# Kernel tuning notes

Measured on AMD Instinct MI355X. Metric: run time of the kernel, lower is better.

## Reference

```python
import jax, jax.numpy as jnp
import numpy as np

KH = KW = 3
K = KH * KW
GROUPS = 8


def conv_same(x, w, b=None):
    out = jax.lax.conv_general_dilated(x, w, (1, 1), 'SAME',
                                       dimension_numbers=('NHWC', 'HWIO', 'NHWC'))
    if b is not None:
        out = out + b
    return out


def feature_selection(x, w_att, w_sel):
    pooled = x.mean(axis=(1, 2), keepdims=True)            # [B,1,1,C]
    attn = jax.nn.sigmoid(conv_same(pooled, w_att))        # 1x1 conv, sigmoid
    return conv_same(x * (attn + 1.0), w_sel)              # [B,H,W,F]


def deform_sample(x, sy, sx):
    # x: [H,W,G,Cg]; sy,sx: [H,W,G,K] fractional sample coords (zero outside)
    H, W, G, _ = x.shape
    y0 = jnp.floor(sy)
    x0 = jnp.floor(sx)
    wy1 = sy - y0
    wx1 = sx - x0
    gi = jnp.arange(G)[None, None, :, None]

    def gather(yi, xi):
        valid = (yi >= 0) & (yi <= H - 1) & (xi >= 0) & (xi <= W - 1)
        yc = jnp.clip(yi, 0, H - 1).astype(jnp.int32)
        xc = jnp.clip(xi, 0, W - 1).astype(jnp.int32)
        v = x[yc, xc, gi]                                   # [H,W,G,K,Cg]
        return v * valid[..., None]

    v00 = gather(y0, x0)
    v01 = gather(y0, x0 + 1)
    v10 = gather(y0 + 1, x0)
    v11 = gather(y0 + 1, x0 + 1)
    wy1 = wy1[..., None]
    wx1 = wx1[..., None]
    top = v00 * (1 - wx1) + v01 * wx1
    bot = v10 * (1 - wx1) + v11 * wx1
    return top * (1 - wy1) + bot * wy1                      # [H,W,G,K,Cg]


def dcnv2(x, align, w_om, b_om, w_dcn, b_dcn):
    # x: [B,H,W,C] input to deform-conv; align: [B,H,W,Ca] alignment feature
    B, H, W, C = x.shape
    G = GROUPS
    Cg = C // G
    om = conv_same(align, w_om, b_om)                       # [B,H,W,G*3*K]
    off = om[..., :G * 2 * K].reshape(B, H, W, G, K, 2)     # (dy, dx)
    mask = jax.nn.sigmoid(om[..., G * 2 * K:]).reshape(B, H, W, G, K)

    iy = jnp.arange(H, dtype=x.dtype)[:, None, None, None]
    ix = jnp.arange(W, dtype=x.dtype)[None, :, None, None]
    ky, kx = jnp.meshgrid(jnp.arange(KH) - (KH - 1) // 2,
                          jnp.arange(KW) - (KW - 1) // 2, indexing='ij')
    ky = ky.reshape(K).astype(x.dtype)
    kx = kx.reshape(K).astype(x.dtype)
    sy = iy + ky + off[..., 0]                              # [B,H,W,G,K]
    sx = ix + kx + off[..., 1]

    xg = x.reshape(B, H, W, G, Cg)
    sampled = jax.vmap(deform_sample)(xg, sy, sx)           # [B,H,W,G,K,Cg]
    sampled = sampled * mask[..., None]
    sampled = sampled.transpose(0, 1, 2, 4, 3, 5).reshape(B, H, W, K, C)
    wk = w_dcn.reshape(K, C, -1)                            # [K,C,F]
    return jnp.einsum('bhwkc,kcf->bhwf', sampled, wk) + b_dcn


def reference(coarse, fine, w_att, w_sel, w_off, w_om, b_om, w_dcn, b_dcn):
    B, H, W, _ = fine.shape
    coarse_up = jax.image.resize(coarse, (B, H, W, coarse.shape[-1]), 'bilinear')
    fine_cal = feature_selection(fine, w_att, w_sel)
    fc = jnp.concatenate([fine_cal, coarse_up * 2.0], axis=-1)
    align = conv_same(fc, w_off)                            # 1x1, no bias
    aligned = jax.nn.relu(dcnv2(coarse_up, align, w_om, b_om, w_dcn, b_dcn))
    return aligned + fine_cal


def setup_inputs() -> dict:
    key = jax.random.key(0)
    ks = jax.random.split(key, 8)
    B, H, W = 4, 64, 64
    Cc, Cf, F = 256, 256, 256
    s = lambda fan: (2.0 / fan) ** 0.5
    return {
        'coarse': jax.random.normal(ks[0], (B, H // 2, W // 2, Cc), jnp.float32),
        'fine': jax.random.normal(ks[1], (B, H, W, Cf), jnp.float32),
        'w_att': jax.random.normal(ks[2], (1, 1, Cf, Cf), jnp.float32) * s(Cf),
        'w_sel': jax.random.normal(ks[3], (1, 1, Cf, F), jnp.float32) * s(Cf),
        'w_off': jax.random.normal(ks[4], (1, 1, F + Cc, 2 * F), jnp.float32) * s(F + Cc),
        'w_om': jax.random.normal(ks[5], (3, 3, 2 * F, GROUPS * 3 * K), jnp.float32) * 0.01,
        'b_om': jnp.zeros((GROUPS * 3 * K,), jnp.float32),
        'w_dcn': jax.random.normal(ks[6], (3, 3, Cc, F), jnp.float32) * s(9 * Cc),
        'b_dcn': jnp.zeros((F,), jnp.float32),
    }
```

## Files before the change

### kernel.cpp

```cpp
#include <hip/hip_runtime.h>
#include <hip/hip_bf16.h>
#include <cstddef>

constexpr int HWP = 64 * 64;
constexpr int CCH = 256;
constexpr int OMC = 216;
constexpr int KDC = 2304;

typedef __attribute__((ext_vector_type(8))) short bf16x8;
typedef __attribute__((ext_vector_type(4))) float f32x4;

__device__ inline unsigned short f2bf(float x) {
  __hip_bfloat16 h = __float2bfloat16(x);
  return *reinterpret_cast<unsigned short*>(&h);
}
__device__ inline float bf2f(unsigned short u) {
  unsigned int v = ((unsigned int)u) << 16;
  return __uint_as_float(v);
}
__device__ inline void bfpair(unsigned int u, float& a, float& b) {
  a = __uint_as_float(u << 16);
  b = __uint_as_float(u & 0xffff0000u);
}

__global__ __launch_bounds__(256) void prep_weights(
    const float* __restrict__ w_off, const float* __restrict__ w_om,
    const float* __restrict__ w_sel, const float* __restrict__ w_dcn,
    unsigned short* __restrict__ w_offT, unsigned short* __restrict__ w_omT,
    unsigned short* __restrict__ w_selT, unsigned short* __restrict__ w_dcnT) {
  int i = blockIdx.x * 256 + threadIdx.x;
  if (i < 512 * 512) {
    int n = i >> 9, k = i & 511;
    w_offT[i] = f2bf(w_off[k * 512 + n]);
  }
  if (i < 9 * 224 * 512) {
    int c = i & 511;
    int r = i >> 9;
    int tap = r / 224;
    int n = r - tap * 224;
    w_omT[i] = f2bf(n < OMC ? w_om[((size_t)tap * 512 + c) * OMC + n] : 0.f);
  }
  if (i < 256 * 256) {
    int n = i >> 8, k = i & 255;
    w_selT[i] = f2bf(w_sel[k * 256 + n]);
  }
  if (i < 9 * 256 * 256) {
    int tap = i >> 16, f = (i >> 8) & 255, c = i & 255;
    w_dcnT[i] = f2bf(w_dcn[((size_t)tap * 256 + c) * 256 + f]);
  }
}

__global__ __launch_bounds__(256) void pool_partial(
    const float* __restrict__ fine, float* __restrict__ partial) {
  int r = blockIdx.x;
  int b = blockIdx.y;
  int t = threadIdx.x;
  const float* src = fine + ((size_t)b * 4096 + r * 64) * 256 + t;
  float s = 0.f;
#pragma unroll 8
  for (int p = 0; p < 64; ++p) s += src[(size_t)p * 256];
  partial[((size_t)b * 64 + r) * 256 + t] = s;
}

__global__ __launch_bounds__(256) void pool_finish(
    const float* __restrict__ partial, const float* __restrict__ w_att,
    float* __restrict__ scale) {
  __shared__ float pl[256];
  int b = blockIdx.x;
  int t = threadIdx.x;
  const float* pp = partial + (size_t)b * 64 * 256 + t;
  float s = 0.f;
#pragma unroll 8
  for (int r = 0; r < 64; ++r) s += pp[(size_t)r * 256];
  pl[t] = s * (1.0f / 4096.0f);
  __syncthreads();
  float acc = 0.f;
  for (int ci = 0; ci < 256; ++ci) acc += pl[ci] * w_att[ci * 256 + t];
  scale[b * 256 + t] = 1.0f + 1.0f / (1.0f + expf(-acc));
}

__global__ __launch_bounds__(256) void upsample_kernel(
    const float* __restrict__ coarse, unsigned short* __restrict__ upbf,
    unsigned short* __restrict__ alignA) {
  int m = blockIdx.x;
  int c = threadIdx.x;
  int b = m >> 12, h = (m >> 6) & 63, w = m & 63;
  float cy = fminf(fmaxf(h * 0.5f - 0.25f, 0.f), 31.f);
  float cx = fminf(fmaxf(w * 0.5f - 0.25f, 0.f), 31.f);
  int y0 = (int)cy, x0 = (int)cx;
  float fy = cy - y0, fx = cx - x0;
  int y1 = min(y0 + 1, 31), x1 = min(x0 + 1, 31);
  const float* base = coarse + (size_t)b * 32 * 32 * CCH;
  float v00 = base[(y0 * 32 + x0) * CCH + c];
  float v01 = base[(y0 * 32 + x1) * CCH + c];
  float v10 = base[(y1 * 32 + x0) * CCH + c];
  float v11 = base[(y1 * 32 + x1) * CCH + c];
  float top = v00 + (v01 - v00) * fx;
  float bot = v10 + (v11 - v10) * fx;
  float v = top + (bot - top) * fy;
  upbf[(size_t)m * CCH + c] = f2bf(v);
  alignA[(size_t)m * 512 + 256 + c] = f2bf(2.f * v);
}

__global__ __launch_bounds__(256) void gemm_finecal_mfma(
    const float* __restrict__ fine, const float* __restrict__ scale,
    const unsigned short* __restrict__ w_selT,
    float* __restrict__ finecal, unsigned short* __restrict__ alignA) {
  __shared__ unsigned short As[128][72];
  __shared__ unsigned short Bs[64][72];
  __shared__ float sc[256];
  int n0 = blockIdx.x * 64;
  int m0 = blockIdx.y * 128;
  int t = threadIdx.x;
  int wid = t >> 6, lane = t & 63;
  int lrow = lane & 15, lq = lane >> 4;
  int bb = m0 >> 12;
  sc[t] = scale[bb * 256 + t];
  f32x4 acc[2][4];
#pragma unroll
  for (int i = 0; i < 2; ++i)
#pragma unroll
    for (int j = 0; j < 4; ++j) acc[i][j] = (f32x4){0.f, 0.f, 0.f, 0.f};
  for (int k0 = 0; k0 < 256; k0 += 64) {
    __syncthreads();
    for (int u = t; u < 128 * 8; u += 256) {
      int row = u >> 3, ck = u & 7;
      const float* fp = &fine[(size_t)(m0 + row) * 256 + k0 + ck * 8];
      float4 f0 = *(const float4*)fp;
      float4 f1 = *(const float4*)(fp + 4);
      int kb = k0 + ck * 8;
      ushort4 u0 = make_ushort4(f2bf(f0.x * sc[kb]), f2bf(f0.y * sc[kb + 1]),
                                f2bf(f0.z * sc[kb + 2]), f2bf(f0.w * sc[kb + 3]));
      ushort4 u1 = make_ushort4(f2bf(f1.x * sc[kb + 4]), f2bf(f1.y * sc[kb + 5]),
                                f2bf(f1.z * sc[kb + 6]), f2bf(f1.w * sc[kb + 7]));
      *(ushort4*)&As[row][ck * 8] = u0;
      *(ushort4*)&As[row][ck * 8 + 4] = u1;
    }
    for (int u = t; u < 64 * 8; u += 256) {
      int row = u >> 3, ck = u & 7;
      *(uint4*)&Bs[row][ck * 8] = *(const uint4*)&w_selT[(size_t)(n0 + row) * 256 + k0 + ck * 8];
    }
    __syncthreads();
#pragma unroll
    for (int kk = 0; kk < 2; ++kk) {
      bf16x8 a[2], b[4];
#pragma unroll
      for (int mt = 0; mt < 2; ++mt)
        a[mt] = *(const bf16x8*)&As[wid * 32 + mt * 16 + lrow][kk * 32 + lq * 8];
#pragma unroll
      for (int nt = 0; nt < 4; ++nt)
        b[nt] = *(const bf16x8*)&Bs[nt * 16 + lrow][kk * 32 + lq * 8];
#pragma unroll
      for (int mt = 0; mt < 2; ++mt)
#pragma unroll
        for (int nt = 0; nt < 4; ++nt)
          acc[mt][nt] = __builtin_amdgcn_mfma_f32_16x16x32_bf16(
              a[mt], b[nt], acc[mt][nt], 0, 0, 0);
    }
  }
#pragma unroll
  for (int mt = 0; mt < 2; ++mt)
#pragma unroll
    for (int nt = 0; nt < 4; ++nt)
#pragma unroll
      for (int r = 0; r < 4; ++r) {
        int m = m0 + wid * 32 + mt * 16 + lq * 4 + r;
        int n = n0 + nt * 16 + lrow;
        finecal[(size_t)m * 256 + n] = acc[mt][nt][r];
        alignA[(size_t)m * 512 + n] = f2bf(acc[mt][nt][r]);
      }
}

__global__ __launch_bounds__(256) void gemm_align_mfma(
    const unsigned short* __restrict__ alignA,
    const unsigned short* __restrict__ w_offT,
    unsigned short* __restrict__ alignBf) {
  __shared__ unsigned short As[128][72];
  __shared__ unsigned short Bs[64][72];
  int n0 = blockIdx.x * 64;
  int m0 = blockIdx.y * 128;
  int t = threadIdx.x;
  int wid = t >> 6, lane = t & 63;
  int lrow = lane & 15, lq = lane >> 4;
  f32x4 acc[2][4];
#pragma unroll
  for (int i = 0; i < 2; ++i)
#pragma unroll
    for (int j = 0; j < 4; ++j) acc[i][j] = (f32x4){0.f, 0.f, 0.f, 0.f};
  for (int k0 = 0; k0 < 512; k0 += 64) {
    __syncthreads();
    for (int u = t; u < 128 * 8; u += 256) {
      int row = u >> 3, ck = u & 7;
      *(uint4*)&As[row][ck * 8] =
          *(const uint4*)&alignA[(size_t)(m0 + row) * 512 + k0 + ck * 8];
    }
    for (int u = t; u < 64 * 8; u += 256) {
      int row = u >> 3, ck = u & 7;
      *(uint4*)&Bs[row][ck * 8] =
          *(const uint4*)&w_offT[(size_t)(n0 + row) * 512 + k0 + ck * 8];
    }
    __syncthreads();
#pragma unroll
    for (int kk = 0; kk < 2; ++kk) {
      bf16x8 a[2], b[4];
#pragma unroll
      for (int mt = 0; mt < 2; ++mt)
        a[mt] = *(const bf16x8*)&As[wid * 32 + mt * 16 + lrow][kk * 32 + lq * 8];
#pragma unroll
      for (int nt = 0; nt < 4; ++nt)
        b[nt] = *(const bf16x8*)&Bs[nt * 16 + lrow][kk * 32 + lq * 8];
#pragma unroll
      for (int mt = 0; mt < 2; ++mt)
#pragma unroll
        for (int nt = 0; nt < 4; ++nt)
          acc[mt][nt] = __builtin_amdgcn_mfma_f32_16x16x32_bf16(
              a[mt], b[nt], acc[mt][nt], 0, 0, 0);
    }
  }
#pragma unroll
  for (int mt = 0; mt < 2; ++mt)
#pragma unroll
    for (int nt = 0; nt < 4; ++nt)
#pragma unroll
      for (int r = 0; r < 4; ++r) {
        int m = m0 + wid * 32 + mt * 16 + lq * 4 + r;
        int n = n0 + nt * 16 + lrow;
        alignBf[(size_t)m * 512 + n] = f2bf(acc[mt][nt][r]);
      }
}

__global__ __launch_bounds__(256) void om_conv_mfma(
    const unsigned short* __restrict__ alignBf,
    const unsigned short* __restrict__ w_omT,
    const float* __restrict__ b_om,
    float* __restrict__ om) {
  __shared__ unsigned short As[3][66][72];
  __shared__ unsigned short Bs[112][72];
  int bh = blockIdx.x;
  int nhalf = blockIdx.y;
  int h = bh & 63;
  int t = threadIdx.x;
  int wid = t >> 6, lane = t & 63;
  int lrow = lane & 15, lq = lane >> 4;
  f32x4 acc[7];
#pragma unroll
  for (int j = 0; j < 7; ++j) acc[j] = (f32x4){0.f, 0.f, 0.f, 0.f};
  for (int c0 = 0; c0 < 512; c0 += 64) {
    __syncthreads();
    for (int u = t; u < 3 * 66 * 8; u += 256) {
      int dy = u / 528;
      int r = u - dy * 528;
      int px = r >> 3, ck = r & 7;
      int w = px - 1;
      int y = h + dy - 1;
      uint4 v = make_uint4(0u, 0u, 0u, 0u);
      if (w >= 0 && w < 64 && y >= 0 && y < 64)
        v = *(const uint4*)&alignBf[((size_t)(bh + dy - 1) * 64 + w) * 512 + c0 + ck * 8];
      *(uint4*)&As[dy][px][ck * 8] = v;
    }
    for (int tap = 0; tap < 9; ++tap) {
      __syncthreads();
      for (int u = t; u < 112 * 8; u += 256) {
        int n = u >> 3, ck = u & 7;
        *(uint4*)&Bs[n][ck * 8] =
            *(const uint4*)&w_omT[((size_t)tap * 224 + nhalf * 112 + n) * 512 + c0 + ck * 8];
      }
      __syncthreads();
      int dyt = tap / 3, dxt = tap - dyt * 3;
#pragma unroll
      for (int kk = 0; kk < 2; ++kk) {
        bf16x8 a = *(const bf16x8*)&As[dyt][wid * 16 + lrow + dxt][kk * 32 + lq * 8];
#pragma unroll
        for (int nt = 0; nt < 7; ++nt) {
          bf16x8 b = *(const bf16x8*)&Bs[nt * 16 + lrow][kk * 32 + lq * 8];
          acc[nt] = __builtin_amdgcn_mfma_f32_16x16x32_bf16(a, b, acc[nt], 0, 0, 0);
        }
      }
    }
  }
#pragma unroll
  for (int nt = 0; nt < 7; ++nt) {
    int n = nhalf * 112 + nt * 16 + lrow;
    if (n < OMC) {
      float bias = b_om[n];
#pragma unroll
      for (int r = 0; r < 4; ++r) {
        int m = bh * 64 + wid * 16 + lq * 4 + r;
        om[(size_t)m * OMC + n] = acc[nt][r] + bias;
      }
    }
  }
}

__global__ __launch_bounds__(256) void dcn_sample(
    const float* __restrict__ om, const unsigned short* __restrict__ upbf,
    unsigned short* __restrict__ S, int bh0) {
  __shared__ int offsA[256][4];
  __shared__ float wtsA[256][4];
  int blk = blockIdx.x;
  int bh = bh0 + (blk >> 1);
  int half = blk & 1;
  int b = bh >> 6, h = bh & 63;
  int p0 = half * 32;
  int m0g = bh * 64 + p0;
  int mloc0 = (bh - bh0) * 64 + p0;
  int t = threadIdx.x;
  const unsigned short* upb = upbf + (size_t)b * HWP * CCH;
  int lane = t & 63;
  int ph = t >> 6;
  int c = lane * 4;
  int g = lane >> 3;
  for (int tap = 0; tap < 9; ++tap) {
    int ky = tap / 3, kx = tap - ky * 3;
    __syncthreads();
    {
      int p = t >> 3, gg = t & 7;
      const float* omr = om + (size_t)(m0g + p) * OMC;
      float dy = omr[gg * 18 + tap * 2];
      float dx = omr[gg * 18 + tap * 2 + 1];
      float mk = 1.0f / (1.0f + expf(-omr[144 + gg * 9 + tap]));
      float sy = (float)(h + ky - 1) + dy;
      float sx = (float)(p0 + p + kx - 1) + dx;
      float y0f = floorf(sy), x0f = floorf(sx);
      float fy = sy - y0f, fx = sx - x0f;
      int y0 = (int)y0f, x0 = (int)x0f;
      int y1 = y0 + 1, x1 = x0 + 1;
      float vy0 = (y0 >= 0 && y0 <= 63) ? 1.f : 0.f;
      float vy1 = (y1 >= 0 && y1 <= 63) ? 1.f : 0.f;
      float vx0 = (x0 >= 0 && x0 <= 63) ? 1.f : 0.f;
      float vx1 = (x1 >= 0 && x1 <= 63) ? 1.f : 0.f;
      int yc0 = min(max(y0, 0), 63), yc1 = min(max(y1, 0), 63);
      int xc0 = min(max(x0, 0), 63), xc1 = min(max(x1, 0), 63);
      offsA[t][0] = (yc0 * 64 + xc0) * 256;
      offsA[t][1] = (yc0 * 64 + xc1) * 256;
      offsA[t][2] = (yc1 * 64 + xc0) * 256;
      offsA[t][3] = (yc1 * 64 + xc1) * 256;
      wtsA[t][0] = (1.f - fy) * (1.f - fx) * vy0 * vx0 * mk;
      wtsA[t][1] = (1.f - fy) * fx * vy0 * vx1 * mk;
      wtsA[t][2] = fy * (1.f - fx) * vy1 * vx0 * mk;
      wtsA[t][3] = fy * fx * vy1 * vx1 * mk;
    }
    __syncthreads();
#pragma unroll
    for (int pp = 0; pp < 8; ++pp) {
      int p = ph * 8 + pp;
      int idx = (p << 3) | g;
      int4 o = *(const int4*)&offsA[idx][0];
      float4 wv = *(const float4*)&wtsA[idx][0];
      uint2 u00 = *(const uint2*)&upb[o.x + c];
      uint2 u01 = *(const uint2*)&upb[o.y + c];
      uint2 u10 = *(const uint2*)&upb[o.z + c];
      uint2 u11 = *(const uint2*)&upb[o.w + c];
      float a0, a1, a2, a3, b0, b1, b2, b3, c0, c1, c2, c3, d0, d1, d2, d3;
      bfpair(u00.x, a0, a1); bfpair(u00.y, a2, a3);
      bfpair(u01.x, b0, b1); bfpair(u01.y, b2, b3);
      bfpair(u10.x, c0, c1); bfpair(u10.y, c2, c3);
      bfpair(u11.x, d0, d1); bfpair(u11.y, d2, d3);
      float v0 = wv.x * a0 + wv.y * b0 + wv.z * c0 + wv.w * d0;
      float v1 = wv.x * a1 + wv.y * b1 + wv.z * c1 + wv.w * d1;
      float v2 = wv.x * a2 + wv.y * b2 + wv.z * c2 + wv.w * d2;
      float v3 = wv.x * a3 + wv.y * b3 + wv.z * c3 + wv.w * d3;
      uint2 outv;
      outv.x = (unsigned int)f2bf(v0) | ((unsigned int)f2bf(v1) << 16);
      outv.y = (unsigned int)f2bf(v2) | ((unsigned int)f2bf(v3) << 16);
      *(uint2*)&S[(size_t)(mloc0 + p) * KDC + tap * 256 + c] = outv;
    }
  }
}

__global__ __launch_bounds__(256) void dcn_gemm(
    const unsigned short* __restrict__ S,
    const unsigned short* __restrict__ w_dcnT,
    const float* __restrict__ b_dcn,
    const float* __restrict__ finecal,
    float* __restrict__ outp, int m_base) {
  __shared__ unsigned short As[128][72];
  __shared__ unsigned short Bs[128][72];
  int n0 = blockIdx.x * 128;
  int mloc0 = blockIdx.y * 128;
  int m0 = m_base + mloc0;
  int t = threadIdx.x;
  int wid = t >> 6, lane = t & 63;
  int wy = wid >> 1, wx = wid & 1;
  int lrow = lane & 15, lq = lane >> 4;
  f32x4 acc[4][4];
#pragma unroll
  for (int i = 0; i < 4; ++i)
#pragma unroll
    for (int j = 0; j < 4; ++j) acc[i][j] = (f32x4){0.f, 0.f, 0.f, 0.f};
  for (int k0 = 0; k0 < KDC; k0 += 64) {
    __syncthreads();
    for (int u = t; u < 128 * 8; u += 256) {
      int row = u >> 3, ck = u & 7;
      *(uint4*)&As[row][ck * 8] =
          *(const uint4*)&S[(size_t)(mloc0 + row) * KDC + k0 + ck * 8];
    }
    int tap = k0 >> 8, c0 = k0 & 255;
    for (int u = t; u < 128 * 8; u += 256) {
      int row = u >> 3, ck = u & 7;
      *(uint4*)&Bs[row][ck * 8] =
          *(const uint4*)&w_dcnT[((size_t)tap * 256 + n0 + row) * 256 + c0 + ck * 8];
    }
    __syncthreads();
#pragma unroll
    for (int kk = 0; kk < 2; ++kk) {
      bf16x8 a[4], b[4];
#pragma unroll
      for (int mt = 0; mt < 4; ++mt)
        a[mt] = *(const bf16x8*)&As[wy * 64 + mt * 16 + lrow][kk * 32 + lq * 8];
#pragma unroll
      for (int nt = 0; nt < 4; ++nt)
        b[nt] = *(const bf16x8*)&Bs[wx * 64 + nt * 16 + lrow][kk * 32 + lq * 8];
#pragma unroll
      for (int mt = 0; mt < 4; ++mt)
#pragma unroll
        for (int nt = 0; nt < 4; ++nt)
          acc[mt][nt] = __builtin_amdgcn_mfma_f32_16x16x32_bf16(
              a[mt], b[nt], acc[mt][nt], 0, 0, 0);
    }
  }
#pragma unroll
  for (int mt = 0; mt < 4; ++mt)
#pragma unroll
    for (int nt = 0; nt < 4; ++nt) {
      int f = n0 + wx * 64 + nt * 16 + lrow;
      float bias = b_dcn[f];
#pragma unroll
      for (int r = 0; r < 4; ++r) {
        int m = m0 + wy * 64 + mt * 16 + lq * 4 + r;
        float v = fmaxf(acc[mt][nt][r] + bias, 0.f);
        float fc = __builtin_nontemporal_load(&finecal[(size_t)m * 256 + f]);
        __builtin_nontemporal_store(v + fc, &outp[(size_t)m * 256 + f]);
      }
    }
}

extern "C" void kernel_launch(void* const* d_in, const int* in_sizes, int n_in,
                              void* d_out, int out_size, void* d_ws, size_t ws_size,
                              hipStream_t stream) {
  const float* coarse = (const float*)d_in[0];
  const float* fine   = (const float*)d_in[1];
  const float* w_att  = (const float*)d_in[2];
  const float* w_sel  = (const float*)d_in[3];
  const float* w_off  = (const float*)d_in[4];
  const float* w_om   = (const float*)d_in[5];
  const float* b_om   = (const float*)d_in[6];
  const float* w_dcn  = (const float*)d_in[7];
  const float* b_dcn  = (const float*)d_in[8];
  float* outp = (float*)d_out;

  char* base = (char*)d_ws;
  size_t o = 0;
  float* scale            = (float*)(base + o);          o += 4096;
  float* finecal          = (float*)(base + o);          o += 16777216;
  float* omb              = (float*)(base + o);          o += 14155776;
  unsigned short* upbf    = (unsigned short*)(base + o); o += 8388608;
  unsigned short* w_offT  = (unsigned short*)(base + o); o += 524288;
  unsigned short* w_omT   = (unsigned short*)(base + o); o += 2064384;
  unsigned short* w_selT  = (unsigned short*)(base + o); o += 131072;
  unsigned short* w_dcnT  = (unsigned short*)(base + o); o += 1179648;
  unsigned short* Sbuf    = (unsigned short*)(base + o);
  size_t fixed = o;
  unsigned short* alignA  = Sbuf;
  unsigned short* alignBf = (unsigned short*)((char*)Sbuf + 16777216);
  float* partial = omb;

  bool fullS = (ws_size >= fixed + 75497472);

  prep_weights<<<dim3(4032), dim3(256), 0, stream>>>(
      w_off, w_om, w_sel, w_dcn, w_offT, w_omT, w_selT, w_dcnT);
  pool_partial<<<dim3(64, 4), dim3(256), 0, stream>>>(fine, partial);
  pool_finish<<<dim3(4), dim3(256), 0, stream>>>(partial, w_att, scale);
  upsample_kernel<<<dim3(16384), dim3(256), 0, stream>>>(coarse, upbf, alignA);
  gemm_finecal_mfma<<<dim3(4, 128), dim3(256), 0, stream>>>(
      fine, scale, w_selT, finecal, alignA);
  gemm_align_mfma<<<dim3(8, 128), dim3(256), 0, stream>>>(alignA, w_offT, alignBf);
  om_conv_mfma<<<dim3(256, 2), dim3(256), 0, stream>>>(alignBf, w_omT, b_om, omb);

  if (fullS) {
    dcn_sample<<<dim3(512), dim3(256), 0, stream>>>(omb, upbf, Sbuf, 0);
    dcn_gemm<<<dim3(2, 128), dim3(256), 0, stream>>>(
        Sbuf, w_dcnT, b_dcn, finecal, outp, 0);
  } else {
    for (int ch = 0; ch < 2; ++ch) {
      dcn_sample<<<dim3(256), dim3(256), 0, stream>>>(omb, upbf, Sbuf, ch * 128);
      dcn_gemm<<<dim3(2, 64), dim3(256), 0, stream>>>(
          Sbuf, w_dcnT, b_dcn, finecal, outp, ch * 8192);
    }
  }
}
```

Measured before the change: 481.9 us.

## Retile offset-mask conv to 128x64 blocks with double-buffered weight staging

The 3x3 offset/mask convolution kernel now tiles two image rows by 64 output channels per block, with a 2x2 warp layout where each warp computes 4x2 MFMA tiles. This replaces one row by 112 channels with a 1x7 layout. The weight tile is double-buffered so the next tap's weights load while the current MFMAs run, which removes one barrier per tap. Output channels are padded to 256, which adds 40 wasted columns in the last block (versus 8 before). The grid shrinks from 512 to 512 blocks of a different shape, and register use rises.

```diff
diff --git a/kernel.cpp b/kernel.cpp
--- a/kernel.cpp
+++ b/kernel.cpp
@@ -33,11 +33,11 @@
     int n = i >> 9, k = i & 511;
     w_offT[i] = f2bf(w_off[k * 512 + n]);
   }
-  if (i < 9 * 224 * 512) {
+  if (i < 9 * 256 * 512) {
     int c = i & 511;
     int r = i >> 9;
-    int tap = r / 224;
-    int n = r - tap * 224;
+    int tap = r >> 8;
+    int n = r & 255;
     w_omT[i] = f2bf(n < OMC ? w_om[((size_t)tap * 512 + c) * OMC + n] : 0.f);
   }
   if (i < 256 * 256) {
@@ -234,59 +234,91 @@
     const unsigned short* __restrict__ w_omT,
     const float* __restrict__ b_om,
     float* __restrict__ om) {
-  __shared__ unsigned short As[3][66][72];
-  __shared__ unsigned short Bs[112][72];
-  int bh = blockIdx.x;
-  int nhalf = blockIdx.y;
-  int h = bh & 63;
+  __shared__ unsigned short As[4][66][72];
+  __shared__ unsigned short Bs[2][64][72];
+  int nblk = blockIdx.x;
+  int mblk = blockIdx.y;
+  int b = mblk >> 5, hp = mblk & 31;
+  int h0 = hp * 2;
+  int n0 = nblk * 64;
   int t = threadIdx.x;
   int wid = t >> 6, lane = t & 63;
+  int wy = wid >> 1, wx = wid & 1;
   int lrow = lane & 15, lq = lane >> 4;
-  f32x4 acc[7];
-#pragma unroll
-  for (int j = 0; j < 7; ++j) acc[j] = (f32x4){0.f, 0.f, 0.f, 0.f};
-  for (int c0 = 0; c0 < 512; c0 += 64) {
-    __syncthreads();
-    for (int u = t; u < 3 * 66 * 8; u += 256) {
+  const size_t imgbase = (size_t)b * 4096;
+  f32x4 acc[4][2];
+#pragma unroll
+  for (int i = 0; i < 4; ++i)
+#pragma unroll
+    for (int j = 0; j < 2; ++j) acc[i][j] = (f32x4){0.f, 0.f, 0.f, 0.f};
+
+  auto stageB = [&](int buf, int tap, int c0) {
+    for (int u = t; u < 64 * 8; u += 256) {
+      int n = u >> 3, ck = u & 7;
+      *(uint4*)&Bs[buf][n][ck * 8] =
+          *(const uint4*)&w_omT[((size_t)tap * 256 + n0 + n) * 512 + c0 * 64 + ck * 8];
+    }
+  };
+  auto stageA = [&](int c0) {
+    for (int u = t; u < 4 * 66 * 8; u += 256) {
       int dy = u / 528;
       int r = u - dy * 528;
       int px = r >> 3, ck = r & 7;
       int w = px - 1;
-      int y = h + dy - 1;
+      int y = h0 - 1 + dy;
       uint4 v = make_uint4(0u, 0u, 0u, 0u);
       if (w >= 0 && w < 64 && y >= 0 && y < 64)
-        v = *(const uint4*)&alignBf[((size_t)(bh + dy - 1) * 64 + w) * 512 + c0 + ck * 8];
+        v = *(const uint4*)&alignBf[(imgbase + y * 64 + w) * 512 + c0 * 64 + ck * 8];
       *(uint4*)&As[dy][px][ck * 8] = v;
     }
+  };
+
+  stageB(0, 0, 0);
+  stageA(0);
+  __syncthreads();
+  int buf = 0;
+  for (int c0 = 0; c0 < 8; ++c0) {
     for (int tap = 0; tap < 9; ++tap) {
-      __syncthreads();
-      for (int u = t; u < 112 * 8; u += 256) {
-        int n = u >> 3, ck = u & 7;
-        *(uint4*)&Bs[n][ck * 8] =
-            *(const uint4*)&w_omT[((size_t)tap * 224 + nhalf * 112 + n) * 512 + c0 + ck * 8];
+      int ntap = tap + 1, nc0 = c0;
+      if (ntap == 9) { ntap = 0; nc0 = (c0 + 1) & 7; }
+      stageB(buf ^ 1, ntap, nc0);
+      int dyt = tap / 3, dxt = tap - dyt * 3;
+#pragma unroll
+      for (int kk = 0; kk < 2; ++kk) {
+        bf16x8 a[4], bb[2];
+#pragma unroll
+        for (int mt = 0; mt < 4; ++mt)
+          a[mt] = *(const bf16x8*)&As[wy + dyt][mt * 16 + lrow + dxt][kk * 32 + lq * 8];
+#pragma unroll
+        for (int nt = 0; nt < 2; ++nt)
+          bb[nt] = *(const bf16x8*)&Bs[buf][wx * 32 + nt * 16 + lrow][kk * 32 + lq * 8];
+#pragma unroll
+        for (int mt = 0; mt < 4; ++mt)
+#pragma unroll
+          for (int nt = 0; nt < 2; ++nt)
+            acc[mt][nt] = __builtin_amdgcn_mfma_f32_16x16x32_bf16(
+                a[mt], bb[nt], acc[mt][nt], 0, 0, 0);
       }
       __syncthreads();
-      int dyt = tap / 3, dxt = tap - dyt * 3;
-#pragma unroll
-      for (int kk = 0; kk < 2; ++kk) {
-        bf16x8 a = *(const bf16x8*)&As[dyt][wid * 16 + lrow + dxt][kk * 32 + lq * 8];
-#pragma unroll
-        for (int nt = 0; nt < 7; ++nt) {
-          bf16x8 b = *(const bf16x8*)&Bs[nt * 16 + lrow][kk * 32 + lq * 8];
-          acc[nt] = __builtin_amdgcn_mfma_f32_16x16x32_bf16(a, b, acc[nt], 0, 0, 0);
-        }
-      }
-    }
-  }
-#pragma unroll
-  for (int nt = 0; nt < 7; ++nt) {
-    int n = nhalf * 112 + nt * 16 + lrow;
+      buf ^= 1;
+    }
+    if (c0 < 7) {
+      stageA(c0 + 1);
+      __syncthreads();
+    }
+  }
+#pragma unroll
+  for (int nt = 0; nt < 2; ++nt) {
+    int n = n0 + wx * 32 + nt * 16 + lrow;
     if (n < OMC) {
       float bias = b_om[n];
 #pragma unroll
-      for (int r = 0; r < 4; ++r) {
-        int m = bh * 64 + wid * 16 + lq * 4 + r;
-        om[(size_t)m * OMC + n] = acc[nt][r] + bias;
+      for (int mt = 0; mt < 4; ++mt) {
+#pragma unroll
+        for (int r = 0; r < 4; ++r) {
+          size_t m = imgbase + (size_t)(h0 + wy) * 64 + mt * 16 + lq * 4 + r;
+          om[m * OMC + n] = acc[mt][nt][r] + bias;
+        }
       }
     }
   }
@@ -456,7 +488,7 @@
   float* omb              = (float*)(base + o);          o += 14155776;
   unsigned short* upbf    = (unsigned short*)(base + o); o += 8388608;
   unsigned short* w_offT  = (unsigned short*)(base + o); o += 524288;
-  unsigned short* w_omT   = (unsigned short*)(base + o); o += 2064384;
+  unsigned short* w_omT   = (unsigned short*)(base + o); o += 2359296;
   unsigned short* w_selT  = (unsigned short*)(base + o); o += 131072;
   unsigned short* w_dcnT  = (unsigned short*)(base + o); o += 1179648;
   unsigned short* Sbuf    = (unsigned short*)(base + o);
@@ -467,7 +499,7 @@
 
   bool fullS = (ws_size >= fixed + 75497472);
 
-  prep_weights<<<dim3(4032), dim3(256), 0, stream>>>(
+  prep_weights<<<dim3(4608), dim3(256), 0, stream>>>(
       w_off, w_om, w_sel, w_dcn, w_offT, w_omT, w_selT, w_dcnT);
   pool_partial<<<dim3(64, 4), dim3(256), 0, stream>>>(fine, partial);
   pool_finish<<<dim3(4), dim3(256), 0, stream>>>(partial, w_att, scale);
@@ -475,7 +507,7 @@
   gemm_finecal_mfma<<<dim3(4, 128), dim3(256), 0, stream>>>(
       fine, scale, w_selT, finecal, alignA);
   gemm_align_mfma<<<dim3(8, 128), dim3(256), 0, stream>>>(alignA, w_offT, alignBf);
-  om_conv_mfma<<<dim3(256, 2), dim3(256), 0, stream>>>(alignBf, w_omT, b_om, omb);
+  om_conv_mfma<<<dim3(4, 128), dim3(256), 0, stream>>>(alignBf, w_omT, b_om, omb);
 
   if (fullS) {
     dcn_sample<<<dim3(512), dim3(256), 0, stream>>>(omb, upbf, Sbuf, 0);
```

Result: faster. 443.3 us (-8.0%).
